# Kernel optimization log

Hardware: AMD Instinct MI355X
Metric: run time of the kernel (lower is better)

The kernel has to match this reference:

```python
import jax, jax.numpy as jnp
import numpy as np

MASS = 60.0


def setup_inputs() -> dict:
    key = jax.random.key(0)
    k1, k2, k3 = jax.random.split(key, 3)
    pre_len, batch, n_nb = 64, 1024, 256
    output = jax.random.normal(k1, (pre_len, batch, 2), dtype=jnp.float32)
    target = jax.random.normal(k2, (pre_len, batch, 2), dtype=jnp.float32)
    # neighbours: [batch, n_nb, 5] = [coord_x, coord_y, v_x, v_y, angle]
    neighbours = jax.random.normal(k3, (batch, n_nb, 5), dtype=jnp.float32)
    return {"output": output, "target": target, "neighbours": neighbours}


def _field_energy(out_bt2, neighbours):
    # out_bt2: [B, T, 2]; neighbours: [B, N, 5]
    nx = neighbours[:, None, :, 0]   # [B, 1, N]
    ny = neighbours[:, None, :, 1]
    ang = neighbours[:, None, :, 4]
    px = out_bt2[:, :, 0][:, :, None]  # [B, T, 1]
    py = out_bt2[:, :, 1][:, :, None]
    dx = px - nx                     # [B, T, N]
    dy = py - ny
    ca, sa = jnp.cos(ang), jnp.sin(ang)
    x_ = ca * dx + sa * dy
    y_ = -sa * dx + ca * dy
    energy_i = MASS / (x_ ** 6 + y_ ** 6 + 6.0)  # [B, T, N]
    nb_angle = jnp.arctan2(-dy, -dx)             # atan2(ny - py, nx - px)
    ex = jnp.sum(energy_i * jnp.cos(nb_angle), axis=-1)  # [B, T]
    ey = jnp.sum(energy_i * jnp.sin(nb_angle), axis=-1)
    energy_norm = jnp.sqrt(ex ** 2 + ey ** 2)    # [B, T]
    # mean over prediction steps per pedestrian, then mean over pedestrians
    return jnp.mean(jnp.mean(energy_norm, axis=1))


def reference(output, target, neighbours):
    loss1 = jnp.mean((output - target) ** 2)  # nn.MSELoss default
    out_bt2 = jnp.transpose(output, (1, 0, 2))  # [B, T, 2]
    field_energy_mean = _field_energy(out_bt2, neighbours)
    return loss1 + field_energy_mean
```

## Files before the change

kernel.cpp:

```cpp
#include <hip/hip_runtime.h>
#include <math.h>

#define PRE_LEN 64
#define BATCH   1024
#define NNB     256

__global__ __launch_bounds__(256, 4) void field_loss_stage1(
    const float* __restrict__ output,
    const float* __restrict__ target,
    const float* __restrict__ nbr,
    float* __restrict__ ws)
{
    __shared__ float4 s_nb[NNB];
    __shared__ float2 s_red[4][64];

    const int b   = blockIdx.x;
    const int tid = threadIdx.x;
    const int t   = tid & 63;
    const int q   = tid >> 6;

    const size_t o_idx = (size_t)t * (BATCH * 2) + (size_t)b * 2;
    const float2 pxy = *reinterpret_cast<const float2*>(&output[o_idx]);
    const float2 txy = *reinterpret_cast<const float2*>(&target[o_idx]);

    {
        const float* p = nbr + ((size_t)b * NNB + tid) * 5;
        const float nx  = p[0];
        const float ny  = p[1];
        const float ang = p[4];
        const float rev = ang * 0.31830988618f;
        const float c2  = __builtin_amdgcn_cosf(rev);
        const float s2  = __builtin_amdgcn_sinf(rev);
        s_nb[tid] = make_float4(nx, ny, c2, 0.5f * s2);
    }
    __syncthreads();

    const float px = pxy.x;
    const float py = pxy.y;

    float ex = 0.0f, ey = 0.0f;
    const int n0 = q * 64;
#pragma unroll 8
    for (int i = 0; i < 64; ++i) {
        const float4 nb = s_nb[n0 + i];
        const float dx  = px - nb.x;
        const float dy  = py - nb.y;
        const float dx2 = dx * dx;
        const float pp  = dx * dy;
        const float r2  = __builtin_fmaf(dy, dy, dx2);
        const float qq  = __builtin_fmaf(-dy, dy, dx2);
        const float t0  = qq * nb.w;
        const float xy  = __builtin_fmaf(pp, nb.z, -t0);
        const float xy2 = xy * xy;
        const float r4  = r2 * r2;
        const float inr = __builtin_fmaf(xy2, -3.0f, r4);
        const float den = __builtin_fmaf(r2, inr, 6.0f);
        const float m2  = den * den * r2;
        const float s   = 60.0f * __builtin_amdgcn_rsqf(m2);
        ex = __builtin_fmaf(s, dx, ex);
        ey = __builtin_fmaf(s, dy, ey);
    }

    s_red[q][t] = make_float2(ex, ey);
    __syncthreads();

    if (q == 0) {
        float tex = 0.0f, tey = 0.0f;
        #pragma unroll
        for (int k = 0; k < 4; ++k) {
            const float2 r = s_red[k][t];
            tex += r.x; tey += r.y;
        }
        const float h2 = __builtin_fmaf(tex, tex, tey * tey);
        const float en = __builtin_amdgcn_sqrtf(h2);

        const float ddx = px - txy.x, ddy = py - txy.y;
        float val = en * (1.0f / (PRE_LEN * BATCH))
                  + (ddx * ddx + ddy * ddy) * (1.0f / (PRE_LEN * BATCH * 2));

        #pragma unroll
        for (int off = 32; off > 0; off >>= 1)
            val += __shfl_down(val, off, 64);

        if (t == 0)
            ws[b] = val;
    }
}

__global__ __launch_bounds__(256) void reduce_kernel(
    const float* __restrict__ ws,
    float* __restrict__ out)
{
    __shared__ float s_part[4];
    const int tid = threadIdx.x;
    const int t   = tid & 63;
    const int q   = tid >> 6;

    float val = ws[tid] + ws[tid + 256] + ws[tid + 512] + ws[tid + 768];

    #pragma unroll
    for (int off = 32; off > 0; off >>= 1)
        val += __shfl_down(val, off, 64);

    if (t == 0) s_part[q] = val;
    __syncthreads();

    if (tid == 0)
        out[0] = s_part[0] + s_part[1] + s_part[2] + s_part[3];
}

extern "C" void kernel_launch(void* const* d_in, const int* in_sizes, int n_in,
                              void* d_out, int out_size, void* d_ws, size_t ws_size,
                              hipStream_t stream) {
    const float* output = (const float*)d_in[0];
    const float* target = (const float*)d_in[1];
    const float* nbr    = (const float*)d_in[2];
    float* out = (float*)d_out;
    float* ws  = (float*)d_ws;

    field_loss_stage1<<<dim3(BATCH), dim3(256), 0, stream>>>(output, target, nbr, ws);
    reduce_kernel<<<dim3(1), dim3(256), 0, stream>>>(ws, out);
}
```

Before: 15.65 us.

## Compute two timesteps per thread to reuse neighbour LDS loads; shrink final reduce

Each thread now handles two prediction timesteps against 32 neighbours instead of one timestep against 64. Every float4 neighbour read from shared memory therefore serves two position evaluations, halving LDS traffic per unit of work and adding independent work for ILP. Partial sums are first combined across half-waves with xor shuffles, then through a float4 shared array. The final reduction becomes a single-wavefront kernel using float4 loads with no shared memory or barrier. This costs more registers per thread and slightly more complex indexing.

```diff
diff --git a/kernel.cpp b/kernel.cpp
--- a/kernel.cpp
+++ b/kernel.cpp
@@ -12,22 +12,27 @@
     float* __restrict__ ws)
 {
     __shared__ float4 s_nb[NNB];
-    __shared__ float2 s_red[4][64];
+    __shared__ float4 s_red[4][32];
 
     const int b   = blockIdx.x;
     const int tid = threadIdx.x;
-    const int t   = tid & 63;
+    const int l   = tid & 63;
     const int q   = tid >> 6;
+    const int p   = l & 31;
+    const int t0  = 2 * p;
 
-    const size_t o_idx = (size_t)t * (BATCH * 2) + (size_t)b * 2;
-    const float2 pxy = *reinterpret_cast<const float2*>(&output[o_idx]);
-    const float2 txy = *reinterpret_cast<const float2*>(&target[o_idx]);
+    const size_t o0 = (size_t)t0 * (BATCH * 2) + (size_t)b * 2;
+    const size_t o1 = o0 + (BATCH * 2);
+    const float2 pxy0 = *reinterpret_cast<const float2*>(&output[o0]);
+    const float2 pxy1 = *reinterpret_cast<const float2*>(&output[o1]);
+    const float2 txy0 = *reinterpret_cast<const float2*>(&target[o0]);
+    const float2 txy1 = *reinterpret_cast<const float2*>(&target[o1]);
 
     {
-        const float* p = nbr + ((size_t)b * NNB + tid) * 5;
-        const float nx  = p[0];
-        const float ny  = p[1];
-        const float ang = p[4];
+        const float* pn = nbr + ((size_t)b * NNB + tid) * 5;
+        const float nx  = pn[0];
+        const float ny  = pn[1];
+        const float ang = pn[4];
         const float rev = ang * 0.31830988618f;
         const float c2  = __builtin_amdgcn_cosf(rev);
         const float s2  = __builtin_amdgcn_sinf(rev);
@@ -35,78 +40,99 @@
     }
     __syncthreads();
 
-    const float px = pxy.x;
-    const float py = pxy.y;
+    const float px0 = pxy0.x, py0 = pxy0.y;
+    const float px1 = pxy1.x, py1 = pxy1.y;
 
-    float ex = 0.0f, ey = 0.0f;
-    const int n0 = q * 64;
-#pragma unroll 8
-    for (int i = 0; i < 64; ++i) {
+    float ex0 = 0.0f, ey0 = 0.0f, ex1 = 0.0f, ey1 = 0.0f;
+    const int n0 = ((l >> 5) + 2 * q) * 32;
+#pragma unroll 4
+    for (int i = 0; i < 32; ++i) {
         const float4 nb = s_nb[n0 + i];
-        const float dx  = px - nb.x;
-        const float dy  = py - nb.y;
-        const float dx2 = dx * dx;
-        const float pp  = dx * dy;
-        const float r2  = __builtin_fmaf(dy, dy, dx2);
-        const float qq  = __builtin_fmaf(-dy, dy, dx2);
-        const float t0  = qq * nb.w;
-        const float xy  = __builtin_fmaf(pp, nb.z, -t0);
-        const float xy2 = xy * xy;
-        const float r4  = r2 * r2;
-        const float inr = __builtin_fmaf(xy2, -3.0f, r4);
-        const float den = __builtin_fmaf(r2, inr, 6.0f);
-        const float m2  = den * den * r2;
-        const float s   = 60.0f * __builtin_amdgcn_rsqf(m2);
-        ex = __builtin_fmaf(s, dx, ex);
-        ey = __builtin_fmaf(s, dy, ey);
+        {
+            const float dx  = px0 - nb.x;
+            const float dy  = py0 - nb.y;
+            const float dx2 = dx * dx;
+            const float pp  = dx * dy;
+            const float r2  = __builtin_fmaf(dy, dy, dx2);
+            const float qq  = __builtin_fmaf(-dy, dy, dx2);
+            const float xy  = __builtin_fmaf(pp, nb.z, -(qq * nb.w));
+            const float inr = __builtin_fmaf(xy * xy, -3.0f, r2 * r2);
+            const float den = __builtin_fmaf(r2, inr, 6.0f);
+            const float s   = 60.0f * __builtin_amdgcn_rsqf(den * den * r2);
+            ex0 = __builtin_fmaf(s, dx, ex0);
+            ey0 = __builtin_fmaf(s, dy, ey0);
+        }
+        {
+            const float dx  = px1 - nb.x;
+            const float dy  = py1 - nb.y;
+            const float dx2 = dx * dx;
+            const float pp  = dx * dy;
+            const float r2  = __builtin_fmaf(dy, dy, dx2);
+            const float qq  = __builtin_fmaf(-dy, dy, dx2);
+            const float xy  = __builtin_fmaf(pp, nb.z, -(qq * nb.w));
+            const float inr = __builtin_fmaf(xy * xy, -3.0f, r2 * r2);
+            const float den = __builtin_fmaf(r2, inr, 6.0f);
+            const float s   = 60.0f * __builtin_amdgcn_rsqf(den * den * r2);
+            ex1 = __builtin_fmaf(s, dx, ex1);
+            ey1 = __builtin_fmaf(s, dy, ey1);
+        }
     }
 
-    s_red[q][t] = make_float2(ex, ey);
+    ex0 += __shfl_xor(ex0, 32, 64);
+    ey0 += __shfl_xor(ey0, 32, 64);
+    ex1 += __shfl_xor(ex1, 32, 64);
+    ey1 += __shfl_xor(ey1, 32, 64);
+
+    if (l < 32)
+        s_red[q][p] = make_float4(ex0, ey0, ex1, ey1);
     __syncthreads();
 
     if (q == 0) {
-        float tex = 0.0f, tey = 0.0f;
+        float tex0 = 0.0f, tey0 = 0.0f, tex1 = 0.0f, tey1 = 0.0f;
         #pragma unroll
         for (int k = 0; k < 4; ++k) {
-            const float2 r = s_red[k][t];
-            tex += r.x; tey += r.y;
+            const float4 r = s_red[k][p];
+            tex0 += r.x; tey0 += r.y; tex1 += r.z; tey1 += r.w;
         }
-        const float h2 = __builtin_fmaf(tex, tex, tey * tey);
-        const float en = __builtin_amdgcn_sqrtf(h2);
+        const float en0 = __builtin_amdgcn_sqrtf(
+            __builtin_fmaf(tex0, tex0, tey0 * tey0));
+        const float en1 = __builtin_amdgcn_sqrtf(
+            __builtin_fmaf(tex1, tex1, tey1 * tey1));
 
-        const float ddx = px - txy.x, ddy = py - txy.y;
-        float val = en * (1.0f / (PRE_LEN * BATCH))
-                  + (ddx * ddx + ddy * ddy) * (1.0f / (PRE_LEN * BATCH * 2));
+        const float d0x = px0 - txy0.x, d0y = py0 - txy0.y;
+        const float d1x = px1 - txy1.x, d1y = py1 - txy1.y;
+
+        float val = (en0 + en1) * (1.0f / (PRE_LEN * BATCH))
+                  + (d0x * d0x + d0y * d0y + d1x * d1x + d1y * d1y)
+                    * (1.0f / (PRE_LEN * BATCH * 2));
 
         #pragma unroll
-        for (int off = 32; off > 0; off >>= 1)
+        for (int off = 16; off > 0; off >>= 1)
             val += __shfl_down(val, off, 64);
 
-        if (t == 0)
+        if (l == 0)
             ws[b] = val;
     }
 }
 
-__global__ __launch_bounds__(256) void reduce_kernel(
-    const float* __restrict__ ws,
+__global__ __launch_bounds__(64) void reduce_kernel(
+    const float4* __restrict__ ws4,
     float* __restrict__ out)
 {
-    __shared__ float s_part[4];
-    const int tid = threadIdx.x;
-    const int t   = tid & 63;
-    const int q   = tid >> 6;
-
-    float val = ws[tid] + ws[tid + 256] + ws[tid + 512] + ws[tid + 768];
+    const int l = threadIdx.x;
+    const float4 a = ws4[l];
+    const float4 b = ws4[l + 64];
+    const float4 c = ws4[l + 128];
+    const float4 d = ws4[l + 192];
+    float v = ((a.x + a.y) + (a.z + a.w)) + ((b.x + b.y) + (b.z + b.w))
+            + ((c.x + c.y) + (c.z + c.w)) + ((d.x + d.y) + (d.z + d.w));
 
     #pragma unroll
     for (int off = 32; off > 0; off >>= 1)
-        val += __shfl_down(val, off, 64);
+        v += __shfl_down(v, off, 64);
 
-    if (t == 0) s_part[q] = val;
-    __syncthreads();
-
-    if (tid == 0)
-        out[0] = s_part[0] + s_part[1] + s_part[2] + s_part[3];
+    if (l == 0)
+        out[0] = v;
 }
 
 extern "C" void kernel_launch(void* const* d_in, const int* in_sizes, int n_in,
@@ -119,5 +145,5 @@
     float* ws  = (float*)d_ws;
 
     field_loss_stage1<<<dim3(BATCH), dim3(256), 0, stream>>>(output, target, nbr, ws);
-    reduce_kernel<<<dim3(1), dim3(256), 0, stream>>>(ws, out);
+    reduce_kernel<<<dim3(1), dim3(64), 0, stream>>>((const float4*)ws, out);
 }
```

Result: no change. 15.76 us (+0.7%).
